# Optimization experiments

Measured on AMD Instinct MI355X. Metric: run time of the kernel, lower is better.

The kernel has to match this reference:

```python
import jax, jax.numpy as jnp
import numpy as np
import math

NUM_HEADS = 8

def _ln(x, g, b, eps=1e-5):
    mu = x.mean(-1, keepdims=True)
    var = ((x - mu) ** 2).mean(-1, keepdims=True)
    return (x - mu) / jnp.sqrt(var + eps) * g + b

def setup_inputs() -> dict:
    key = jax.random.key(0)
    ks = jax.random.split(key, 10)
    B, Nq, Nk, dQ, dK, dV = 16, 1024, 1024, 512, 512, 512
    s = 0.05  # small init so the double-exp in masked_softmax stays finite
    Q = jax.random.normal(ks[0], (B, Nq, dQ), jnp.float32)
    K = jax.random.normal(ks[1], (B, Nk, dK), jnp.float32)
    Qm = (jax.random.uniform(ks[2], (B, Nq, 1)) < 0.9).astype(jnp.float32)
    Km = (jax.random.uniform(ks[3], (B, Nk, 1)) < 0.9).astype(jnp.float32)
    Wq = jax.random.normal(ks[4], (dQ, dV), jnp.float32) * s
    Wk = jax.random.normal(ks[5], (dK, dV), jnp.float32) * s
    Wv = jax.random.normal(ks[6], (dK, dV), jnp.float32) * s
    Wo = jax.random.normal(ks[7], (dV, dV), jnp.float32) * s
    bq = jnp.zeros((dV,), jnp.float32); bk = jnp.zeros((dV,), jnp.float32)
    bv = jnp.zeros((dV,), jnp.float32); bo = jnp.zeros((dV,), jnp.float32)
    g0 = jnp.ones((dV,), jnp.float32); b0 = jnp.zeros((dV,), jnp.float32)
    g1 = jnp.ones((dV,), jnp.float32); b1 = jnp.zeros((dV,), jnp.float32)
    return {"Q": Q, "K": K, "Qm": Qm, "Km": Km,
            "Wq": Wq, "bq": bq, "Wk": Wk, "bk": bk, "Wv": Wv, "bv": bv,
            "Wo": Wo, "bo": bo, "g0": g0, "b0": b0, "g1": g1, "b1": b1}

def reference(Q, K, Qm, Km, Wq, bq, Wk, bk, Wv, bv, Wo, bo, g0, b0, g1, b1):
    B, Nq, _ = Q.shape
    Nk = K.shape[1]
    dV = Wq.shape[1]
    h = NUM_HEADS
    dh = dV // h
    # projections + feature masking (Qm/Km broadcast over feature dim)
    Qp = (Q @ Wq + bq) * Qm          # [B,Nq,dV]
    Kp = (K @ Wk + bk) * Km          # [B,Nk,dV]
    V  = K @ Wv + bv                 # [B,Nk,dV]
    # head split: torch.cat(split(dh,2),0) == head-major [h,B,N,dh]
    Qh = Qp.reshape(B, Nq, h, dh).transpose(2, 0, 1, 3)
    Kh = Kp.reshape(B, Nk, h, dh).transpose(2, 0, 1, 3)
    Vh = V.reshape(B, Nk, h, dh).transpose(2, 0, 1, 3)
    S = jnp.einsum('hbqd,hbkd->hbqk', Qh, Kh) / math.sqrt(dV)
    # faithful masked_softmax: exp applied twice (Km branch then Qm branch)
    X = jnp.exp(S) * Km[:, :, 0][None, :, None, :]   # [h,B,Nq,Nk]
    X = jnp.exp(X) * Qm[:, :, 0][None, :, :, None]
    A = X / (X.sum(-1, keepdims=True) + 1e-8)
    O = Qh + jnp.einsum('hbqk,hbkd->hbqd', A, Vh)    # residual in head space
    O = O.transpose(1, 2, 0, 3).reshape(B, Nq, dV)   # merge heads back
    O = _ln(O, g0, b0)
    O = O + jax.nn.relu(O @ Wo + bo)
    return _ln(O, g1, b1)
```

## Files before the change

kernel.cpp:

```cpp
#include <hip/hip_runtime.h>
#include <hip/hip_bf16.h>
#include <cstdint>


typedef __bf16 bf16;
typedef __bf16 bf16x4 __attribute__((ext_vector_type(4)));
typedef __bf16 bf16x8 __attribute__((ext_vector_type(8)));
typedef float f32x4 __attribute__((ext_vector_type(4)));

#define MFMA16(a, b, c) __builtin_amdgcn_mfma_f32_16x16x32_bf16((a), (b), (c), 0, 0, 0)

#if __has_builtin(__builtin_amdgcn_exp2f)
#define EXP2F(x) __builtin_amdgcn_exp2f(x)
#else
#define EXP2F(x) exp2f(x)
#endif

static __device__ __forceinline__ void async_lds16(const bf16* g, bf16* l) {
  __builtin_amdgcn_global_load_lds(
      (__attribute__((address_space(1))) void*)(void*)g,
      (__attribute__((address_space(3))) void*)l,
      16, 0, 0);
}

static __device__ __forceinline__ void swz512(int id, long& rowBase, int& colBase) {
  colBase = ((id >> 3) & 3) * 128;
  rowBase = (long)((id & 7) + 8 * (id >> 5)) * 128;
}

__global__ __launch_bounds__(256) void transposeW(
    const float* __restrict__ Wq, const float* __restrict__ Wk,
    const float* __restrict__ Wv, const float* __restrict__ Wo,
    bf16* __restrict__ Tq, bf16* __restrict__ Tk,
    bf16* __restrict__ Tv, bf16* __restrict__ To) {
  const float* src;
  bf16* dst;
  switch (blockIdx.z) {
    case 0: src = Wq; dst = Tq; break;
    case 1: src = Wk; dst = Tk; break;
    case 2: src = Wv; dst = Tv; break;
    default: src = Wo; dst = To; break;
  }
  __shared__ bf16 t[64][72];
  const int tid = threadIdx.x;
  const int n0 = blockIdx.x * 64;
  const int k0 = blockIdx.y * 64;
  for (int c = tid; c < 512; c += 256) {
    const int row = c >> 3, col = (c & 7) * 8;
    const float* sp = src + (size_t)(k0 + row) * 512 + n0 + col;
    const f32x4 a = *(const f32x4*)sp;
    const f32x4 b = *(const f32x4*)(sp + 4);
    bf16x8 v;
#pragma unroll
    for (int j = 0; j < 4; ++j) { v[j] = (bf16)a[j]; v[j + 4] = (bf16)b[j]; }
    *(bf16x8*)(&t[row][col]) = v;
  }
  __syncthreads();
  for (int c = tid; c < 512; c += 256) {
    const int row = c >> 3, col8 = (c & 7) * 8;
    bf16x8 v;
#pragma unroll
    for (int j = 0; j < 8; ++j) v[j] = t[col8 + j][row];
    *(bf16x8*)(dst + (size_t)(n0 + row) * 512 + k0 + col8) = v;
  }
}

__global__ __launch_bounds__(256) void convertX(
    const float* __restrict__ Q, const float* __restrict__ K,
    bf16* __restrict__ Qb, bf16* __restrict__ Kb) {
  const float* s = blockIdx.y ? K : Q;
  bf16* d = blockIdx.y ? Kb : Qb;
  const long i = ((long)blockIdx.x * 256 + threadIdx.x) * 8;
  const f32x4 x0 = *(const f32x4*)(s + i);
  const f32x4 x1 = *(const f32x4*)(s + i + 4);
  bf16x8 o;
#pragma unroll
  for (int j = 0; j < 4; ++j) { o[j] = (bf16)x0[j]; o[j + 4] = (bf16)x1[j]; }
  *(bf16x8*)(d + i) = o;
}

struct ConvArgs {
  const float* src[10];
  bf16* dst[10];
  int n[10];
};

__global__ __launch_bounds__(256) void convert_all(ConvArgs a) {
  const int seg = blockIdx.z;
  const int n = a.n[seg];
  const long i = ((long)blockIdx.x * 256 + threadIdx.x) * 8;
  if (i >= n) return;
  const float* s = a.src[seg];
  const f32x4 x0 = *(const f32x4*)(s + i);
  const f32x4 x1 = *(const f32x4*)(s + i + 4);
  bf16x8 o;
#pragma unroll
  for (int j = 0; j < 4; ++j) { o[j] = (bf16)x0[j]; o[j + 4] = (bf16)x1[j]; }
  *(bf16x8*)(a.dst[seg] + i) = o;
}

__global__ __launch_bounds__(256, 2) void gemm512(
    const bf16* __restrict__ A, const bf16* __restrict__ Bt,
    const bf16* __restrict__ bias, const bf16* __restrict__ mask,
    const bf16* __restrict__ resid, bf16* __restrict__ out) {
  __shared__ bf16 sA[128 * 32];
  __shared__ bf16 sB[128 * 32];
  const int tid = threadIdx.x;
  const int lane = tid & 63;
  const int w = tid >> 6;
  const int fm = lane & 15;
  const int fq = lane >> 4;
  long rowBase; int colBase;
  swz512(blockIdx.x, rowBase, colBase);

  f32x4 acc[4][4] = {};

  const int c0 = tid, c1 = tid + 256;
  const int r0 = c0 >> 2, o0 = (c0 & 3) * 8;
  const int r1 = c1 >> 2, o1 = (c1 & 3) * 8;
  const bf16* A0 = A + (rowBase + r0) * 512 + o0;
  const bf16* A1 = A + (rowBase + r1) * 512 + o1;
  const bf16* B0 = Bt + (size_t)(colBase + r0) * 512 + o0;
  const bf16* B1 = Bt + (size_t)(colBase + r1) * 512 + o1;

  const int wr = (w & 1) * 64;
  const int wc = (w >> 1) * 64;

  for (int kt = 0; kt < 16; ++kt) {
    const int k0 = kt * 32;
    __syncthreads();
    async_lds16(A0 + k0, sA + c0 * 8);
    async_lds16(A1 + k0, sA + c1 * 8);
    async_lds16(B0 + k0, sB + c0 * 8);
    async_lds16(B1 + k0, sB + c1 * 8);
    __syncthreads();
    bf16x8 a[4], b[4];
#pragma unroll
    for (int i = 0; i < 4; ++i)
      a[i] = *(const bf16x8*)(sA + (wr + i * 16 + fm) * 32 + fq * 8);
#pragma unroll
    for (int j = 0; j < 4; ++j)
      b[j] = *(const bf16x8*)(sB + (wc + j * 16 + fm) * 32 + fq * 8);
#pragma unroll
    for (int i = 0; i < 4; ++i)
#pragma unroll
      for (int j = 0; j < 4; ++j)
        acc[i][j] = MFMA16(a[i], b[j], acc[i][j]);
  }

#pragma unroll
  for (int i = 0; i < 4; ++i) {
#pragma unroll
    for (int r = 0; r < 4; ++r) {
      const long R = rowBase + wr + i * 16 + fq * 4 + r;
      const float mk = mask ? (float)mask[R] : 1.0f;
      const bf16* resrow = resid ? resid + R * 512 : nullptr;
      bf16* outrow = out + R * 512;
#pragma unroll
      for (int j = 0; j < 4; ++j) {
        const int C = colBase + wc + j * 16 + fm;
        float v = acc[i][j][r] + (float)bias[C];
        if (mask) v *= mk;
        if (resid) v = (float)resrow[C] + fmaxf(v, 0.0f);
        outrow[C] = (bf16)v;
      }
    }
  }
}

__global__ __launch_bounds__(256, 2) void gemmKV(
    const bf16* __restrict__ A, const bf16* __restrict__ Btk,
    const bf16* __restrict__ Btv, const bf16* __restrict__ bk,
    const bf16* __restrict__ bv, const bf16* __restrict__ Km,
    bf16* __restrict__ Kp, bf16* __restrict__ Vt) {
  __shared__ bf16 sA[128 * 32];
  __shared__ bf16 sBk[128 * 32];
  __shared__ bf16 sBv[128 * 32];
  const int tid = threadIdx.x;
  const int lane = tid & 63;
  const int w = tid >> 6;
  const int fm = lane & 15;
  const int fq = lane >> 4;
  long rowBase; int colBase;
  swz512(blockIdx.x, rowBase, colBase);

  f32x4 acck[4][4] = {};
  f32x4 accv[4][4] = {};

  const int c0 = tid, c1 = tid + 256;
  const int r0 = c0 >> 2, o0 = (c0 & 3) * 8;
  const int r1 = c1 >> 2, o1 = (c1 & 3) * 8;
  const bf16* A0 = A + (rowBase + r0) * 512 + o0;
  const bf16* A1 = A + (rowBase + r1) * 512 + o1;
  const bf16* Bk0 = Btk + (size_t)(colBase + r0) * 512 + o0;
  const bf16* Bk1 = Btk + (size_t)(colBase + r1) * 512 + o1;
  const bf16* Bv0 = Btv + (size_t)(colBase + r0) * 512 + o0;
  const bf16* Bv1 = Btv + (size_t)(colBase + r1) * 512 + o1;

  const int wr = (w & 1) * 64;
  const int wc = (w >> 1) * 64;

  for (int kt = 0; kt < 16; ++kt) {
    const int k0 = kt * 32;
    __syncthreads();
    async_lds16(A0 + k0, sA + c0 * 8);
    async_lds16(A1 + k0, sA + c1 * 8);
    async_lds16(Bk0 + k0, sBk + c0 * 8);
    async_lds16(Bk1 + k0, sBk + c1 * 8);
    async_lds16(Bv0 + k0, sBv + c0 * 8);
    async_lds16(Bv1 + k0, sBv + c1 * 8);
    __syncthreads();
    bf16x8 a[4], b[4], bv2[4];
#pragma unroll
    for (int i = 0; i < 4; ++i)
      a[i] = *(const bf16x8*)(sA + (wr + i * 16 + fm) * 32 + fq * 8);
#pragma unroll
    for (int j = 0; j < 4; ++j) {
      b[j] = *(const bf16x8*)(sBk + (wc + j * 16 + fm) * 32 + fq * 8);
      bv2[j] = *(const bf16x8*)(sBv + (wc + j * 16 + fm) * 32 + fq * 8);
    }
#pragma unroll
    for (int i = 0; i < 4; ++i)
#pragma unroll
      for (int j = 0; j < 4; ++j) {
        acck[i][j] = MFMA16(a[i], b[j], acck[i][j]);
        accv[i][j] = MFMA16(a[i], bv2[j], accv[i][j]);
      }
  }

  const int bidx = (int)(rowBase >> 10);
#pragma unroll
  for (int i = 0; i < 4; ++i) {
#pragma unroll
    for (int r = 0; r < 4; ++r) {
      const long R = rowBase + wr + i * 16 + fq * 4 + r;
      const float mk = (float)Km[R];
      bf16* outrow = Kp + R * 512;
#pragma unroll
      for (int j = 0; j < 4; ++j) {
        const int C = colBase + wc + j * 16 + fm;
        outrow[C] = (bf16)((acck[i][j][r] + (float)bk[C]) * mk);
      }
    }
    const int kkb = (int)(rowBase & 1023) + wr + i * 16 + fq * 4;
#pragma unroll
    for (int j = 0; j < 4; ++j) {
      const int C = colBase + wc + j * 16 + fm;
      const float bvc = (float)bv[C];
      bf16x4 pv;
#pragma unroll
      for (int r = 0; r < 4; ++r) pv[r] = (bf16)(accv[i][j][r] + bvc);
      bf16* dst = Vt + ((size_t)(bidx * 8 + (C >> 6)) * 64 + (C & 63)) * 1024 + kkb;
      *(bf16x4*)((void*)dst) = pv;
    }
  }
}

__global__ __launch_bounds__(256, 4) void attn_kernel(
    bf16* __restrict__ Qp, const bf16* __restrict__ Kp,
    const bf16* __restrict__ Vt, const bf16* __restrict__ Qm,
    const bf16* __restrict__ Km) {
  __shared__ bf16 sK[64][72];
  __shared__ bf16 sVt[64][72];
  __shared__ bf16 sX[4][32][72];
  __shared__ float sKl[64];
  __shared__ float sL[4][32];

  const int tid = threadIdx.x;
  const int lane = tid & 63;
  const int w = tid >> 6;
  const int fm = lane & 15;
  const int fq = lane >> 4;
  const int id = blockIdx.x;
  const int bh = id & 127;
  const int q0 = (id >> 7) * 128;
  const int b = bh >> 3;
  const int hh = bh & 7;

  bf16* Qbase = Qp + ((long)b * 1024 + q0) * 512 + hh * 64;
  float qm_lane[2];
  qm_lane[0] = (float)Qm[(long)b * 1024 + q0 + w * 32 + fm];
  qm_lane[1] = (float)Qm[(long)b * 1024 + q0 + w * 32 + 16 + fm];

  bf16x8 qf[2][2];
#pragma unroll
  for (int u = 0; u < 2; ++u)
#pragma unroll
    for (int ks = 0; ks < 2; ++ks)
      qf[u][ks] = *(const bf16x8*)(Qbase + (long)(w * 32 + u * 16 + fm) * 512 +
                                   ks * 32 + fq * 8);

  f32x4 acc_o[2][4] = {};
  float l_lane[2] = {0.f, 0.f};
  const float c1 = 0.063758715f;
  const float LOG2E = 1.4426950408889634f;

  const bf16* Vthead = Vt + ((long)b * 8 + hh) * 64 * 1024;
  const bf16* Kbb = Kp + (long)b * 1024 * 512 + hh * 64;
  const bf16* Kmb = Km + (long)b * 1024;

  for (int kt = 0; kt < 16; ++kt) {
    const int kk0 = kt * 64;
    __syncthreads();
    const bf16* Kbase = Kbb + (long)kk0 * 512;
    for (int c = tid; c < 512; c += 256) {
      const int row = c >> 3, col = (c & 7) * 8;
      *(bf16x8*)(&sK[row][col]) = *(const bf16x8*)(Kbase + (long)row * 512 + col);
      *(bf16x8*)(&sVt[row][col]) =
          *(const bf16x8*)(Vthead + (long)row * 1024 + kk0 + col);
    }
    if (tid < 64) sKl[tid] = (float)Kmb[kk0 + tid] * LOG2E;
    __syncthreads();

    f32x4 s_acc[2][4] = {};
#pragma unroll
    for (int ks = 0; ks < 2; ++ks)
#pragma unroll
      for (int t = 0; t < 4; ++t) {
        const bf16x8 kf = *(const bf16x8*)(&sK[t * 16 + fm][ks * 32 + fq * 8]);
        s_acc[0][t] = MFMA16(kf, qf[0][ks], s_acc[0][t]);
        s_acc[1][t] = MFMA16(kf, qf[1][ks], s_acc[1][t]);
      }
#pragma unroll
    for (int u = 0; u < 2; ++u)
#pragma unroll
      for (int t = 0; t < 4; ++t) {
        const f32x4 kml4 = *(const f32x4*)(&sKl[t * 16 + fq * 4]);
        bf16x4 xp;
#pragma unroll
        for (int r = 0; r < 4; ++r) {
          const float e1 = EXP2F(s_acc[u][t][r] * c1);
          const float y = EXP2F(e1 * kml4[r]);
          l_lane[u] += y;
          xp[r] = (bf16)y;
        }
        *(bf16x4*)((void*)&sX[w][u * 16 + fm][t * 16 + fq * 4]) = xp;
      }
#pragma unroll
    for (int ks = 0; ks < 2; ++ks) {
      const bf16x8 xf0 = *(const bf16x8*)(&sX[w][fm][ks * 32 + fq * 8]);
      const bf16x8 xf1 = *(const bf16x8*)(&sX[w][16 + fm][ks * 32 + fq * 8]);
#pragma unroll
      for (int t = 0; t < 4; ++t) {
        const bf16x8 vf = *(const bf16x8*)(&sVt[t * 16 + fm][ks * 32 + fq * 8]);
        acc_o[0][t] = MFMA16(xf0, vf, acc_o[0][t]);
        acc_o[1][t] = MFMA16(xf1, vf, acc_o[1][t]);
      }
    }
  }

#pragma unroll
  for (int u = 0; u < 2; ++u) {
    l_lane[u] += __shfl_xor(l_lane[u], 16);
    l_lane[u] += __shfl_xor(l_lane[u], 32);
    if (fq == 0) sL[w][u * 16 + fm] = l_lane[u];
  }
  __syncthreads();

#pragma unroll
  for (int u = 0; u < 2; ++u) {
#pragma unroll
    for (int t = 0; t < 4; ++t) {
#pragma unroll
      for (int r = 0; r < 4; ++r) {
        const int qr = w * 32 + u * 16 + fq * 4 + r;
        const int dc = t * 16 + fm;
        const float qm_r = __shfl(qm_lane[u], fq * 4 + r, 64);
        const float li = 1.0f / (qm_r * sL[w][u * 16 + fq * 4 + r] + 1e-8f);
        const float val =
            (float)Qbase[(long)qr * 512 + dc] + qm_r * acc_o[u][t][r] * li;
        Qbase[(long)qr * 512 + dc] = (bf16)val;
      }
    }
  }
}

__global__ __launch_bounds__(256) void lnorm(
    const bf16* __restrict__ X, const bf16* __restrict__ g,
    const bf16* __restrict__ bb, bf16* __restrict__ out) {
  const int row = blockIdx.x * 4 + (threadIdx.x >> 6);
  const int lane = threadIdx.x & 63;
  const bf16x8 v = *(const bf16x8*)(X + (size_t)row * 512 + lane * 8);
  float x[8], s = 0.f, ss = 0.f;
#pragma unroll
  for (int j = 0; j < 8; ++j) {
    x[j] = (float)v[j];
    s += x[j];
    ss += x[j] * x[j];
  }
#pragma unroll
  for (int m = 1; m < 64; m <<= 1) {
    s += __shfl_xor(s, m);
    ss += __shfl_xor(ss, m);
  }
  const float mean = s * (1.0f / 512.0f);
  const float var = ss * (1.0f / 512.0f) - mean * mean;
  const float rstd = 1.0f / sqrtf(var + 1e-5f);
  const bf16x8 gv = *(const bf16x8*)(g + lane * 8);
  const bf16x8 bv = *(const bf16x8*)(bb + lane * 8);
  bf16x8 o;
#pragma unroll
  for (int j = 0; j < 8; ++j)
    o[j] = (bf16)((x[j] - mean) * rstd * (float)gv[j] + (float)bv[j]);
  *(bf16x8*)(out + (size_t)row * 512 + lane * 8) = o;
}

__global__ __launch_bounds__(256) void lnorm_out(
    const bf16* __restrict__ X, const bf16* __restrict__ g,
    const bf16* __restrict__ bb, float* __restrict__ out) {
  const int row = blockIdx.x * 4 + (threadIdx.x >> 6);
  const int lane = threadIdx.x & 63;
  const bf16x8 v = *(const bf16x8*)(X + (size_t)row * 512 + lane * 8);
  float x[8], s = 0.f, ss = 0.f;
#pragma unroll
  for (int j = 0; j < 8; ++j) {
    x[j] = (float)v[j];
    s += x[j];
    ss += x[j] * x[j];
  }
#pragma unroll
  for (int m = 1; m < 64; m <<= 1) {
    s += __shfl_xor(s, m);
    ss += __shfl_xor(ss, m);
  }
  const float mean = s * (1.0f / 512.0f);
  const float var = ss * (1.0f / 512.0f) - mean * mean;
  const float rstd = 1.0f / sqrtf(var + 1e-5f);
  const bf16x8 gv = *(const bf16x8*)(g + lane * 8);
  const bf16x8 bv = *(const bf16x8*)(bb + lane * 8);
  f32x4 a, c;
#pragma unroll
  for (int j = 0; j < 4; ++j) {
    a[j] = (x[j] - mean) * rstd * (float)gv[j] + (float)bv[j];
    c[j] = (x[j + 4] - mean) * rstd * (float)gv[j + 4] + (float)bv[j + 4];
  }
  float* fo = out + (size_t)row * 512 + lane * 8;
  *(f32x4*)fo = a;
  *(f32x4*)(fo + 4) = c;
}

extern "C" void kernel_launch(void* const* d_in, const int* in_sizes, int n_in,
                              void* d_out, int out_size, void* d_ws, size_t ws_size,
                              hipStream_t stream) {
  (void)in_sizes; (void)n_in; (void)out_size; (void)ws_size;
  const float* Q = (const float*)d_in[0];
  const float* K = (const float*)d_in[1];

  bf16* ws = (bf16*)d_ws;
  const long W2 = 512L * 512;
  const long MN = 16384L * 512;
  bf16* Tq = ws;
  bf16* Tk = Tq + W2;
  bf16* Tv = Tk + W2;
  bf16* To = Tv + W2;
  bf16* sm = To + W2;
  bf16* cQm = sm + 8 * 512;
  bf16* cKm = cQm + 16384;
  bf16* Qp = cKm + 16384;
  bf16* Kp = Qp + MN;
  bf16* Qbf = Kp;
  bf16* Kbf = (bf16*)d_out;
  bf16* Vt = (bf16*)d_out + MN;

  bf16* cbq = sm + 0 * 512;
  bf16* cbk = sm + 1 * 512;
  bf16* cbv = sm + 2 * 512;
  bf16* cbo = sm + 3 * 512;
  bf16* cg0 = sm + 4 * 512;
  bf16* cb0 = sm + 5 * 512;
  bf16* cg1 = sm + 6 * 512;
  bf16* cb1 = sm + 7 * 512;

  transposeW<<<dim3(8, 8, 4), 256, 0, stream>>>(
      (const float*)d_in[4], (const float*)d_in[6],
      (const float*)d_in[8], (const float*)d_in[10], Tq, Tk, Tv, To);

  ConvArgs ca;
  ca.src[0] = (const float*)d_in[2];  ca.dst[0] = cQm; ca.n[0] = 16384;
  ca.src[1] = (const float*)d_in[3];  ca.dst[1] = cKm; ca.n[1] = 16384;
  ca.src[2] = (const float*)d_in[5];  ca.dst[2] = cbq; ca.n[2] = 512;
  ca.src[3] = (const float*)d_in[7];  ca.dst[3] = cbk; ca.n[3] = 512;
  ca.src[4] = (const float*)d_in[9];  ca.dst[4] = cbv; ca.n[4] = 512;
  ca.src[5] = (const float*)d_in[11]; ca.dst[5] = cbo; ca.n[5] = 512;
  ca.src[6] = (const float*)d_in[12]; ca.dst[6] = cg0; ca.n[6] = 512;
  ca.src[7] = (const float*)d_in[13]; ca.dst[7] = cb0; ca.n[7] = 512;
  ca.src[8] = (const float*)d_in[14]; ca.dst[8] = cg1; ca.n[8] = 512;
  ca.src[9] = (const float*)d_in[15]; ca.dst[9] = cb1; ca.n[9] = 512;
  convert_all<<<dim3(8, 1, 10), 256, 0, stream>>>(ca);

  convertX<<<dim3(4096, 2), 256, 0, stream>>>(Q, K, Qbf, Kbf);

  gemm512<<<512, 256, 0, stream>>>(Qbf, Tq, cbq, cQm, nullptr, Qp);
  gemmKV<<<512, 256, 0, stream>>>(Kbf, Tk, Tv, cbk, cbv, cKm, Kp, Vt);

  attn_kernel<<<1024, 256, 0, stream>>>(Qp, Kp, Vt, cQm, cKm);

  lnorm<<<4096, 256, 0, stream>>>(Qp, cg0, cb0, Qp);
  gemm512<<<512, 256, 0, stream>>>(Qp, To, cbo, nullptr, Qp, Kp);
  lnorm_out<<<4096, 256, 0, stream>>>(Kp, cg1, cb1, (float*)d_out);
}
```

Before: 290.4 us.

## Fuse fp32-to-bf16 input conversion into projection GEMM loads; add MFMA priority hints

Removes the separate convertX pass over Q and K. The Q and KV projection GEMMs now read fp32 activations directly, convert them to bf16 in registers and store them to LDS, which saves a full write and re-read of a bf16 copy. This costs synchronous global loads in place of async LDS loads for the A operand, and each N-tile re-reads the fp32 data at twice the byte width. Separately, the attention kernel raises wave priority with s_setprio around its MFMA phases.

```diff
diff --git a/kernel.cpp b/kernel.cpp
--- a/kernel.cpp
+++ b/kernel.cpp
@@ -63,20 +63,6 @@
     for (int j = 0; j < 8; ++j) v[j] = t[col8 + j][row];
     *(bf16x8*)(dst + (size_t)(n0 + row) * 512 + k0 + col8) = v;
   }
-}
-
-__global__ __launch_bounds__(256) void convertX(
-    const float* __restrict__ Q, const float* __restrict__ K,
-    bf16* __restrict__ Qb, bf16* __restrict__ Kb) {
-  const float* s = blockIdx.y ? K : Q;
-  bf16* d = blockIdx.y ? Kb : Qb;
-  const long i = ((long)blockIdx.x * 256 + threadIdx.x) * 8;
-  const f32x4 x0 = *(const f32x4*)(s + i);
-  const f32x4 x1 = *(const f32x4*)(s + i + 4);
-  bf16x8 o;
-#pragma unroll
-  for (int j = 0; j < 4; ++j) { o[j] = (bf16)x0[j]; o[j + 4] = (bf16)x1[j]; }
-  *(bf16x8*)(d + i) = o;
 }
 
 struct ConvArgs {
@@ -168,8 +154,85 @@
   }
 }
 
-__global__ __launch_bounds__(256, 2) void gemmKV(
-    const bf16* __restrict__ A, const bf16* __restrict__ Btk,
+__global__ __launch_bounds__(256, 2) void gemm512_f32A(
+    const float* __restrict__ A, const bf16* __restrict__ Bt,
+    const bf16* __restrict__ bias, const bf16* __restrict__ mask,
+    bf16* __restrict__ out) {
+  __shared__ bf16 sA[128 * 32];
+  __shared__ bf16 sB[128 * 32];
+  const int tid = threadIdx.x;
+  const int lane = tid & 63;
+  const int w = tid >> 6;
+  const int fm = lane & 15;
+  const int fq = lane >> 4;
+  long rowBase; int colBase;
+  swz512(blockIdx.x, rowBase, colBase);
+
+  f32x4 acc[4][4] = {};
+
+  const int c0 = tid, c1 = tid + 256;
+  const int r0 = c0 >> 2, o0 = (c0 & 3) * 8;
+  const int r1 = c1 >> 2, o1 = (c1 & 3) * 8;
+  const float* A0 = A + (rowBase + r0) * 512 + o0;
+  const float* A1 = A + (rowBase + r1) * 512 + o1;
+  const bf16* B0 = Bt + (size_t)(colBase + r0) * 512 + o0;
+  const bf16* B1 = Bt + (size_t)(colBase + r1) * 512 + o1;
+
+  const int wr = (w & 1) * 64;
+  const int wc = (w >> 1) * 64;
+
+  for (int kt = 0; kt < 16; ++kt) {
+    const int k0 = kt * 32;
+    __syncthreads();
+    async_lds16(B0 + k0, sB + c0 * 8);
+    async_lds16(B1 + k0, sB + c1 * 8);
+    {
+      const f32x4 x0 = *(const f32x4*)(A0 + k0);
+      const f32x4 x1 = *(const f32x4*)(A0 + k0 + 4);
+      const f32x4 y0 = *(const f32x4*)(A1 + k0);
+      const f32x4 y1 = *(const f32x4*)(A1 + k0 + 4);
+      bf16x8 va, vb;
+#pragma unroll
+      for (int j = 0; j < 4; ++j) {
+        va[j] = (bf16)x0[j]; va[j + 4] = (bf16)x1[j];
+        vb[j] = (bf16)y0[j]; vb[j + 4] = (bf16)y1[j];
+      }
+      *(bf16x8*)(sA + c0 * 8) = va;
+      *(bf16x8*)(sA + c1 * 8) = vb;
+    }
+    __syncthreads();
+    bf16x8 a[4], b[4];
+#pragma unroll
+    for (int i = 0; i < 4; ++i)
+      a[i] = *(const bf16x8*)(sA + (wr + i * 16 + fm) * 32 + fq * 8);
+#pragma unroll
+    for (int j = 0; j < 4; ++j)
+      b[j] = *(const bf16x8*)(sB + (wc + j * 16 + fm) * 32 + fq * 8);
+#pragma unroll
+    for (int i = 0; i < 4; ++i)
+#pragma unroll
+      for (int j = 0; j < 4; ++j)
+        acc[i][j] = MFMA16(a[i], b[j], acc[i][j]);
+  }
+
+#pragma unroll
+  for (int i = 0; i < 4; ++i) {
+#pragma unroll
+    for (int r = 0; r < 4; ++r) {
+      const long R = rowBase + wr + i * 16 + fq * 4 + r;
+      const float mk = (float)mask[R];
+      bf16* outrow = out + R * 512;
+#pragma unroll
+      for (int j = 0; j < 4; ++j) {
+        const int C = colBase + wc + j * 16 + fm;
+        outrow[C] = (bf16)((acc[i][j][r] + (float)bias[C]) * mk);
+      }
+    }
+  }
+}
+
+__global__ __launch_bounds__(256, 2) void gemmKV_f32A(
+    const float* __restrict__ A, const bf16* __restrict__ Btk,
     const bf16* __restrict__ Btv, const bf16* __restrict__ bk,
     const bf16* __restrict__ bv, const bf16* __restrict__ Km,
     bf16* __restrict__ Kp, bf16* __restrict__ Vt) {
@@ -190,8 +253,8 @@
   const int c0 = tid, c1 = tid + 256;
   const int r0 = c0 >> 2, o0 = (c0 & 3) * 8;
   const int r1 = c1 >> 2, o1 = (c1 & 3) * 8;
-  const bf16* A0 = A + (rowBase + r0) * 512 + o0;
-  const bf16* A1 = A + (rowBase + r1) * 512 + o1;
+  const float* A0 = A + (rowBase + r0) * 512 + o0;
+  const float* A1 = A + (rowBase + r1) * 512 + o1;
   const bf16* Bk0 = Btk + (size_t)(colBase + r0) * 512 + o0;
   const bf16* Bk1 = Btk + (size_t)(colBase + r1) * 512 + o1;
   const bf16* Bv0 = Btv + (size_t)(colBase + r0) * 512 + o0;
@@ -203,12 +266,24 @@
   for (int kt = 0; kt < 16; ++kt) {
     const int k0 = kt * 32;
     __syncthreads();
-    async_lds16(A0 + k0, sA + c0 * 8);
-    async_lds16(A1 + k0, sA + c1 * 8);
     async_lds16(Bk0 + k0, sBk + c0 * 8);
     async_lds16(Bk1 + k0, sBk + c1 * 8);
     async_lds16(Bv0 + k0, sBv + c0 * 8);
     async_lds16(Bv1 + k0, sBv + c1 * 8);
+    {
+      const f32x4 x0 = *(const f32x4*)(A0 + k0);
+      const f32x4 x1 = *(const f32x4*)(A0 + k0 + 4);
+      const f32x4 y0 = *(const f32x4*)(A1 + k0);
+      const f32x4 y1 = *(const f32x4*)(A1 + k0 + 4);
+      bf16x8 va, vb;
+#pragma unroll
+      for (int j = 0; j < 4; ++j) {
+        va[j] = (bf16)x0[j]; va[j + 4] = (bf16)x1[j];
+        vb[j] = (bf16)y0[j]; vb[j + 4] = (bf16)y1[j];
+      }
+      *(bf16x8*)(sA + c0 * 8) = va;
+      *(bf16x8*)(sA + c1 * 8) = vb;
+    }
     __syncthreads();
     bf16x8 a[4], b[4], bv2[4];
 #pragma unroll
@@ -313,6 +388,7 @@
     __syncthreads();
 
     f32x4 s_acc[2][4] = {};
+    __builtin_amdgcn_s_setprio(1);
 #pragma unroll
     for (int ks = 0; ks < 2; ++ks)
 #pragma unroll
@@ -321,6 +397,7 @@
         s_acc[0][t] = MFMA16(kf, qf[0][ks], s_acc[0][t]);
         s_acc[1][t] = MFMA16(kf, qf[1][ks], s_acc[1][t]);
       }
+    __builtin_amdgcn_s_setprio(0);
 #pragma unroll
     for (int u = 0; u < 2; ++u)
 #pragma unroll
@@ -336,6 +413,7 @@
         }
         *(bf16x4*)((void*)&sX[w][u * 16 + fm][t * 16 + fq * 4]) = xp;
       }
+    __builtin_amdgcn_s_setprio(1);
 #pragma unroll
     for (int ks = 0; ks < 2; ++ks) {
       const bf16x8 xf0 = *(const bf16x8*)(&sX[w][fm][ks * 32 + fq * 8]);
@@ -347,6 +425,7 @@
         acc_o[1][t] = MFMA16(xf1, vf, acc_o[1][t]);
       }
     }
+    __builtin_amdgcn_s_setprio(0);
   }
 
 #pragma unroll
@@ -458,8 +537,6 @@
   bf16* cKm = cQm + 16384;
   bf16* Qp = cKm + 16384;
   bf16* Kp = Qp + MN;
-  bf16* Qbf = Kp;
-  bf16* Kbf = (bf16*)d_out;
   bf16* Vt = (bf16*)d_out + MN;
 
   bf16* cbq = sm + 0 * 512;
@@ -488,10 +565,8 @@
   ca.src[9] = (const float*)d_in[15]; ca.dst[9] = cb1; ca.n[9] = 512;
   convert_all<<<dim3(8, 1, 10), 256, 0, stream>>>(ca);
 
-  convertX<<<dim3(4096, 2), 256, 0, stream>>>(Q, K, Qbf, Kbf);
-
-  gemm512<<<512, 256, 0, stream>>>(Qbf, Tq, cbq, cQm, nullptr, Qp);
-  gemmKV<<<512, 256, 0, stream>>>(Kbf, Tk, Tv, cbk, cbv, cKm, Kp, Vt);
+  gemm512_f32A<<<512, 256, 0, stream>>>(Q, Tq, cbq, cQm, Qp);
+  gemmKV_f32A<<<512, 256, 0, stream>>>(K, Tk, Tv, cbk, cbv, cKm, Kp, Vt);
 
   attn_kernel<<<1024, 256, 0, stream>>>(Qp, Kp, Vt, cQm, cKm);
 
```

Result: slower. 296.3 us (+2.0%).
